# Optimization experiments

Measured on AMD Instinct MI355X. Metric: run time of the kernel, lower is better.

## Reference

```python
import jax, jax.numpy as jnp
import numpy as np

N_NODES = 50000
N_EDGES = 800000
D = 128
N_GRAPHS = 64


def setup_inputs() -> dict:
    key = jax.random.key(0)
    ks = jax.random.split(key, 10)
    x = jax.random.normal(ks[0], (N_NODES, D), dtype=jnp.float32)
    edge_weight = jax.random.uniform(ks[1], (N_EDGES,), dtype=jnp.float32)
    W1 = jax.random.normal(ks[2], (D, D), dtype=jnp.float32) / np.sqrt(D)
    b1 = jax.random.normal(ks[3], (D,), dtype=jnp.float32) * 0.01
    W2 = jax.random.normal(ks[4], (D, D), dtype=jnp.float32) / np.sqrt(D)
    b2 = jax.random.normal(ks[5], (D,), dtype=jnp.float32) * 0.01
    Wh = jax.random.normal(ks[6], (D, 1), dtype=jnp.float32) / np.sqrt(D)
    bh = jax.random.normal(ks[7], (1,), dtype=jnp.float32) * 0.01
    edge_index = jax.random.randint(ks[8], (2, N_EDGES), 0, N_NODES, dtype=jnp.int64)
    batch = jnp.sort(jax.random.randint(ks[9], (N_NODES,), 0, N_GRAPHS, dtype=jnp.int64))
    return {"x": x, "edge_weight": edge_weight, "W1": W1, "b1": b1,
            "W2": W2, "b2": b2, "Wh": Wh, "bh": bh,
            "edge_index": edge_index, "batch": batch}


def reference(x, edge_weight, W1, b1, W2, b2, Wh, bh, edge_index, batch):
    N = x.shape[0]
    # --- GCN normalization with self-loops (computed once; shared by layers) ---
    row, col = edge_index[0], edge_index[1]
    loop = jnp.arange(N, dtype=edge_index.dtype)
    row2 = jnp.concatenate([row, loop])   # source nodes
    col2 = jnp.concatenate([col, loop])   # target nodes
    ew2 = jnp.concatenate([edge_weight, jnp.ones((N,), dtype=x.dtype)])
    deg = jax.ops.segment_sum(ew2, col2, num_segments=N)
    dinv = jnp.where(deg > 0, jax.lax.rsqrt(deg), 0.0)
    norm = dinv[row2] * ew2 * dinv[col2]  # [E+N]

    def gcn_conv(h, W, b):
        h = h @ W                                   # [N, D_out]
        msg = norm[:, None] * h[row2]               # gather + scale, [E+N, D_out]
        return jax.ops.segment_sum(msg, col2, num_segments=N) + b

    # dropout is identity in eval mode
    h = jax.nn.relu(gcn_conv(x, W1, b1))
    h = jax.nn.relu(gcn_conv(h, W2, b2))

    # --- global mean pool over graphs ---
    counts = jax.ops.segment_sum(jnp.ones((N,), dtype=h.dtype), batch, num_segments=N_GRAPHS)
    pooled = jax.ops.segment_sum(h, batch, num_segments=N_GRAPHS)
    pooled = pooled / jnp.maximum(counts, 1.0)[:, None]
    return pooled @ Wh + bh
```

## Files before the change

### kernel.cpp

```cpp
#include <hip/hip_runtime.h>
#include <hip/hip_bf16.h>
#include <hip/hip_fp16.h>

#define N_NODES  50000
#define N_EDGES  800000
#define D        128
#define N_GRAPHS 64
#define CAP      64
#define EW_SCALE 1048576.0f
#define NB_GEMM1 391
#define NB_FILL  3125
#define NB_AGG16 3125

typedef _Float16 half8 __attribute__((ext_vector_type(8)));
typedef float   float4v __attribute__((ext_vector_type(4)));

__device__ __forceinline__ float2 h2f(unsigned int u) {
    __half2 h = *reinterpret_cast<__half2*>(&u);
    return __half22float2(h);
}
__device__ __forceinline__ unsigned int f2h(float a, float b) {
    __half2 h = __floats2half2_rn(a, b);
    return *reinterpret_cast<unsigned int*>(&h);
}
__device__ __forceinline__ float hu2f(unsigned short u) {
    __half_raw hr; hr.x = u;
    return __half2float(__half(hr));
}
__device__ __forceinline__ void unpack_pd(unsigned long long p, int& n, float& dv) {
    int c = (int)(p >> 40);
    n = c < CAP ? c : CAP;
    dv = rsqrtf(1.0f + (float)(p & 0xFFFFFFFFFFULL) * (1.0f / EW_SCALE));
}

__global__ __launch_bounds__(256) void fused_gemm1_fill(const float* __restrict__ X,
                                                        const float* __restrict__ W,
                                                        __half* __restrict__ Yh,
                                                        const int* __restrict__ ei,
                                                        const float* __restrict__ ew,
                                                        unsigned long long* __restrict__ packed,
                                                        unsigned int* __restrict__ bucket) {
    __shared__ float XT[32 * 128];
    __shared__ float Ws[32 * 128];

    if (blockIdx.x >= NB_GEMM1) {
        int e = (blockIdx.x - NB_GEMM1) * 256 + threadIdx.x;
        if (e >= N_EDGES) return;
        int r = ei[e];
        int c = ei[N_EDGES + e];
        float w = ew[e];
        unsigned long long add = (1ULL << 40) | (unsigned long long)(unsigned)(w * EW_SCALE + 0.5f);
        unsigned long long old = atomicAdd(&packed[c], add);
        unsigned pos = (unsigned)(old >> 40);
        if (pos < CAP) {
            unsigned short wh = __half_as_ushort(__float2half_rn(w));
            bucket[(size_t)c * CAP + pos] = (unsigned)r | ((unsigned)wh << 16);
        }
        return;
    }

    const int tid  = threadIdx.x;
    const int row0 = blockIdx.x * 128;
    const int tr = tid >> 4, tc = tid & 15;
    float acc[8][8] = {};

    for (int kt = 0; kt < 4; kt++) {
        const int kbase = kt * 32;
        {
            const float4* src = (const float4*)(W + kbase * 128);
            float4* dst = (float4*)Ws;
            for (int i = tid; i < 1024; i += 256) dst[i] = src[i];
        }
        {
            int r  = tid >> 1;
            int rr = row0 + r; if (rr >= N_NODES) rr = N_NODES - 1;
            int k0 = (tid & 1) * 16;
            const float4* src = (const float4*)(X + (size_t)rr * 128 + kbase + k0);
#pragma unroll
            for (int i = 0; i < 4; i++) {
                float4 v = src[i];
                int k = k0 + i * 4;
                XT[(k + 0) * 128 + r] = v.x;
                XT[(k + 1) * 128 + r] = v.y;
                XT[(k + 2) * 128 + r] = v.z;
                XT[(k + 3) * 128 + r] = v.w;
            }
        }
        __syncthreads();
#pragma unroll 4
        for (int k = 0; k < 32; k++) {
            float xs[8], ws[8];
            *(float4*)&xs[0] = *(const float4*)(XT + k * 128 + tr * 8);
            *(float4*)&xs[4] = *(const float4*)(XT + k * 128 + tr * 8 + 4);
            *(float4*)&ws[0] = *(const float4*)(Ws + k * 128 + tc * 8);
            *(float4*)&ws[4] = *(const float4*)(Ws + k * 128 + tc * 8 + 4);
#pragma unroll
            for (int i = 0; i < 8; i++)
#pragma unroll
                for (int j = 0; j < 8; j++)
                    acc[i][j] += xs[i] * ws[j];
        }
        __syncthreads();
    }
#pragma unroll
    for (int i = 0; i < 8; i++) {
        int r = row0 + tr * 8 + i;
        if (r < N_NODES) {
            uint4 p;
            p.x = f2h(acc[i][0], acc[i][1]);
            p.y = f2h(acc[i][2], acc[i][3]);
            p.z = f2h(acc[i][4], acc[i][5]);
            p.w = f2h(acc[i][6], acc[i][7]);
            *(uint4*)(Yh + (size_t)r * 128 + tc * 8) = p;
        }
    }
}

__global__ __launch_bounds__(512) void agg1_gemm2_kernel(const __half* __restrict__ xw1,
                                                         const unsigned long long* __restrict__ packed,
                                                         const unsigned int* __restrict__ bucket,
                                                         const float* __restrict__ b1,
                                                         const float* __restrict__ W2,
                                                         __half* __restrict__ x2) {
    __shared__ _Float16 sh1[16][136];
    const int wv   = threadIdx.x >> 6;
    const int lane = threadIdx.x & 63;
    const unsigned int* xh = (const unsigned int*)xw1;
    const int node0 = blockIdx.x * 16;

    float2 bb = ((const float2*)b1)[lane];

#pragma unroll
    for (int j = 0; j < 2; j++) {
        int node = node0 + wv * 2 + j;
        int n; float dv;
        unpack_pd(packed[node], n, dv);

        unsigned pk = 0u;
        if (lane < n) {
            unsigned eh = bucket[(size_t)node * CAP + lane];
            int src = eh & 0xFFFFu;
            int sn; float sdv;
            unpack_pd(packed[src], sn, sdv);
            float v = hu2f((unsigned short)(eh >> 16)) * sdv;
            pk = (unsigned)src | ((unsigned)__half_as_ushort(__float2half_rn(v)) << 16);
        }
        int pki = (int)pk;

        float2 xs = h2f(xh[(size_t)node * 64 + lane]);
        float accx = dv * xs.x;
        float accy = dv * xs.y;

        int i = 0;
        for (; i + 3 < n; i += 4) {
            unsigned v0u = (unsigned)__shfl(pki, i);
            unsigned v1u = (unsigned)__shfl(pki, i + 1);
            unsigned v2u = (unsigned)__shfl(pki, i + 2);
            unsigned v3u = (unsigned)__shfl(pki, i + 3);
            int r0 = v0u & 0xFFFF, r1 = v1u & 0xFFFF, r2 = v2u & 0xFFFF, r3 = v3u & 0xFFFF;
            float v0 = hu2f((unsigned short)(v0u >> 16));
            float v1 = hu2f((unsigned short)(v1u >> 16));
            float v2 = hu2f((unsigned short)(v2u >> 16));
            float v3 = hu2f((unsigned short)(v3u >> 16));
            float2 f0 = h2f(xh[(size_t)r0 * 64 + lane]);
            float2 f1 = h2f(xh[(size_t)r1 * 64 + lane]);
            float2 f2 = h2f(xh[(size_t)r2 * 64 + lane]);
            float2 f3 = h2f(xh[(size_t)r3 * 64 + lane]);
            accx += v0 * f0.x + v1 * f1.x + v2 * f2.x + v3 * f3.x;
            accy += v0 * f0.y + v1 * f1.y + v2 * f2.y + v3 * f3.y;
        }
        for (; i < n; i++) {
            unsigned v0u = (unsigned)__shfl(pki, i);
            int r0 = v0u & 0xFFFF;
            float v0 = hu2f((unsigned short)(v0u >> 16));
            float2 f0 = h2f(xh[(size_t)r0 * 64 + lane]);
            accx += v0 * f0.x;
            accy += v0 * f0.y;
        }

        float hx = fmaxf(dv * accx + bb.x, 0.0f);
        float hy = fmaxf(dv * accy + bb.y, 0.0f);
        int lr = wv * 2 + j;
        sh1[lr][lane * 2]     = (_Float16)hx;
        sh1[lr][lane * 2 + 1] = (_Float16)hy;
    }
    __syncthreads();

    const int quad = lane >> 4;
    const int l16  = lane & 15;
    float4v acc0 = {};
#pragma unroll
    for (int kc = 0; kc < 4; kc++) {
        const int k0 = kc * 32;
        half8 a = *(const half8*)(&sh1[l16][k0 + quad * 8]);
        const float* wp = W2 + (size_t)(k0 + quad * 8) * 128 + wv * 16 + l16;
        half8 b;
#pragma unroll
        for (int jj = 0; jj < 8; jj++) b[jj] = (_Float16)wp[jj * 128];
        acc0 = __builtin_amdgcn_mfma_f32_16x16x32_f16(a, b, acc0, 0, 0, 0);
    }
#pragma unroll
    for (int r = 0; r < 4; r++) {
        int row = node0 + quad * 4 + r;
        int rn; float s;
        unpack_pd(packed[row], rn, s);
        x2[(size_t)row * 128 + wv * 16 + l16] = __float2half_rn(acc0[r] * s);
    }
}

__global__ __launch_bounds__(256) void agg_head_kernel(const __half* __restrict__ xwh,
                                                       const unsigned long long* __restrict__ packed,
                                                       const unsigned int* __restrict__ bucket,
                                                       const float* __restrict__ bias,
                                                       const float* __restrict__ Wh,
                                                       float* __restrict__ nodedot) {
    int node = blockIdx.x * 4 + (threadIdx.x >> 6);
    int lane = threadIdx.x & 63;
    const unsigned int* xh = (const unsigned int*)xwh;

    int n; float dv;
    unpack_pd(packed[node], n, dv);

    unsigned int ehdr = (lane < n) ? bucket[(size_t)node * CAP + lane] : 0u;
    int eh = (int)ehdr;

    float2 xs = h2f(xh[(size_t)node * 64 + lane]);
    float accx = xs.x;
    float accy = xs.y;

    int i = 0;
    for (; i + 3 < n; i += 4) {
        unsigned v0u = (unsigned)__shfl(eh, i);
        unsigned v1u = (unsigned)__shfl(eh, i + 1);
        unsigned v2u = (unsigned)__shfl(eh, i + 2);
        unsigned v3u = (unsigned)__shfl(eh, i + 3);
        int r0 = v0u & 0xFFFF, r1 = v1u & 0xFFFF, r2 = v2u & 0xFFFF, r3 = v3u & 0xFFFF;
        float v0 = hu2f((unsigned short)(v0u >> 16));
        float v1 = hu2f((unsigned short)(v1u >> 16));
        float v2 = hu2f((unsigned short)(v2u >> 16));
        float v3 = hu2f((unsigned short)(v3u >> 16));
        float2 f0 = h2f(xh[(size_t)r0 * 64 + lane]);
        float2 f1 = h2f(xh[(size_t)r1 * 64 + lane]);
        float2 f2 = h2f(xh[(size_t)r2 * 64 + lane]);
        float2 f3 = h2f(xh[(size_t)r3 * 64 + lane]);
        accx += v0 * f0.x + v1 * f1.x + v2 * f2.x + v3 * f3.x;
        accy += v0 * f0.y + v1 * f1.y + v2 * f2.y + v3 * f3.y;
    }
    for (; i < n; i++) {
        unsigned v0u = (unsigned)__shfl(eh, i);
        int r0 = v0u & 0xFFFF;
        float v0 = hu2f((unsigned short)(v0u >> 16));
        float2 f0 = h2f(xh[(size_t)r0 * 64 + lane]);
        accx += v0 * f0.x;
        accy += v0 * f0.y;
    }

    float2 b = ((const float2*)bias)[lane];
    float hx = fmaxf(dv * accx + b.x, 0.0f);
    float hy = fmaxf(dv * accy + b.y, 0.0f);
    float2 w = ((const float2*)Wh)[lane];
    float s = hx * w.x + hy * w.y;
#pragma unroll
    for (int off = 32; off > 0; off >>= 1) s += __shfl_down(s, off, 64);
    if (lane == 0) nodedot[node] = s;
}

__global__ __launch_bounds__(256) void final2_kernel(const float* __restrict__ nodedot,
                                                     const int* __restrict__ batch,
                                                     const float* __restrict__ bh,
                                                     float* __restrict__ out) {
    __shared__ float red[256];
    int g = blockIdx.x;
    int lo = 0, hi = N_NODES;
    while (lo < hi) { int mid = (lo + hi) >> 1; if (batch[mid] < g) lo = mid + 1; else hi = mid; }
    int a = lo;
    hi = N_NODES;
    while (lo < hi) { int mid = (lo + hi) >> 1; if (batch[mid] < g + 1) lo = mid + 1; else hi = mid; }
    int b = lo;

    float s = 0.0f;
    for (int n = a + threadIdx.x; n < b; n += 256) s += nodedot[n];
    red[threadIdx.x] = s;
    __syncthreads();
#pragma unroll
    for (int off = 128; off > 0; off >>= 1) {
        if (threadIdx.x < off) red[threadIdx.x] += red[threadIdx.x + off];
        __syncthreads();
    }
    if (threadIdx.x == 0)
        out[g] = red[0] / fmaxf((float)(b - a), 1.0f) + bh[0];
}

extern "C" void kernel_launch(void* const* d_in, const int* in_sizes, int n_in,
                              void* d_out, int out_size, void* d_ws, size_t ws_size,
                              hipStream_t stream) {
    const float* x   = (const float*)d_in[0];
    const float* ew  = (const float*)d_in[1];
    const float* W1  = (const float*)d_in[2];
    const float* b1  = (const float*)d_in[3];
    const float* W2  = (const float*)d_in[4];
    const float* b2  = (const float*)d_in[5];
    const float* Wh  = (const float*)d_in[6];
    const float* bh  = (const float*)d_in[7];
    const int*   ei  = (const int*)d_in[8];
    const int*   bat = (const int*)d_in[9];
    float* out = (float*)d_out;

    char* ws = (char*)d_ws;
    __half* bufAh  = (__half*)ws;                         ws += (size_t)N_NODES * D * 2;
    __half* bufBh  = (__half*)ws;                         ws += (size_t)N_NODES * D * 2;
    unsigned int* bucket = (unsigned int*)ws;             ws += (size_t)N_NODES * CAP * 4;
    unsigned long long* packed = (unsigned long long*)ws; ws += (size_t)N_NODES * 8;
    float*  nodedot = (float*)ws;                         ws += (size_t)N_NODES * 4;

    const int nb_agg4 = N_NODES / 4;

    hipMemsetAsync(packed, 0, (size_t)N_NODES * 8, stream);

    fused_gemm1_fill<<<NB_GEMM1 + NB_FILL, 256, 0, stream>>>(x, W1, bufAh, ei, ew, packed, bucket);

    agg1_gemm2_kernel<<<NB_AGG16, 512, 0, stream>>>(bufAh, packed, bucket, b1, W2, bufBh);

    agg_head_kernel<<<nb_agg4, 256, 0, stream>>>(bufBh, packed, bucket, b2, Wh, nodedot);

    final2_kernel<<<N_GRAPHS, 256, 0, stream>>>(nodedot, bat, bh, out);
}
```

Measured before the change: 225.9 us.

## Use MFMA f16 for first GEMM and unroll gather loops by eight

The first GEMM, which used an FP32 shared-memory outer-product tile, now runs on MFMA 16x16x32 f16. Each wave handles 16 rows, converts X and W1 to half in registers, and uses no shared memory, so the GEMM block count doubles. Separately, both aggregation loops are unrolled from 4 to 8 neighbours to keep more gathers in flight. The costs are f16 rounding of X and W1 inputs, strided uncoalesced W loads repeated per wave, and more register pressure in the unrolled gathers.

```diff
diff --git a/kernel.cpp b/kernel.cpp
--- a/kernel.cpp
+++ b/kernel.cpp
@@ -8,7 +8,7 @@
 #define N_GRAPHS 64
 #define CAP      64
 #define EW_SCALE 1048576.0f
-#define NB_GEMM1 391
+#define NB_G1M   782
 #define NB_FILL  3125
 #define NB_AGG16 3125
 
@@ -18,10 +18,6 @@
 __device__ __forceinline__ float2 h2f(unsigned int u) {
     __half2 h = *reinterpret_cast<__half2*>(&u);
     return __half22float2(h);
-}
-__device__ __forceinline__ unsigned int f2h(float a, float b) {
-    __half2 h = __floats2half2_rn(a, b);
-    return *reinterpret_cast<unsigned int*>(&h);
 }
 __device__ __forceinline__ float hu2f(unsigned short u) {
     __half_raw hr; hr.x = u;
@@ -40,11 +36,8 @@
                                                         const float* __restrict__ ew,
                                                         unsigned long long* __restrict__ packed,
                                                         unsigned int* __restrict__ bucket) {
-    __shared__ float XT[32 * 128];
-    __shared__ float Ws[32 * 128];
-
-    if (blockIdx.x >= NB_GEMM1) {
-        int e = (blockIdx.x - NB_GEMM1) * 256 + threadIdx.x;
+    if (blockIdx.x >= NB_G1M) {
+        int e = (blockIdx.x - NB_G1M) * 256 + threadIdx.x;
         if (e >= N_EDGES) return;
         int r = ei[e];
         int c = ei[N_EDGES + e];
@@ -59,59 +52,40 @@
         return;
     }
 
-    const int tid  = threadIdx.x;
-    const int row0 = blockIdx.x * 128;
-    const int tr = tid >> 4, tc = tid & 15;
-    float acc[8][8] = {};
-
-    for (int kt = 0; kt < 4; kt++) {
-        const int kbase = kt * 32;
-        {
-            const float4* src = (const float4*)(W + kbase * 128);
-            float4* dst = (float4*)Ws;
-            for (int i = tid; i < 1024; i += 256) dst[i] = src[i];
-        }
-        {
-            int r  = tid >> 1;
-            int rr = row0 + r; if (rr >= N_NODES) rr = N_NODES - 1;
-            int k0 = (tid & 1) * 16;
-            const float4* src = (const float4*)(X + (size_t)rr * 128 + kbase + k0);
-#pragma unroll
-            for (int i = 0; i < 4; i++) {
-                float4 v = src[i];
-                int k = k0 + i * 4;
-                XT[(k + 0) * 128 + r] = v.x;
-                XT[(k + 1) * 128 + r] = v.y;
-                XT[(k + 2) * 128 + r] = v.z;
-                XT[(k + 3) * 128 + r] = v.w;
-            }
-        }
-        __syncthreads();
-#pragma unroll 4
-        for (int k = 0; k < 32; k++) {
-            float xs[8], ws[8];
-            *(float4*)&xs[0] = *(const float4*)(XT + k * 128 + tr * 8);
-            *(float4*)&xs[4] = *(const float4*)(XT + k * 128 + tr * 8 + 4);
-            *(float4*)&ws[0] = *(const float4*)(Ws + k * 128 + tc * 8);
-            *(float4*)&ws[4] = *(const float4*)(Ws + k * 128 + tc * 8 + 4);
-#pragma unroll
-            for (int i = 0; i < 8; i++)
-#pragma unroll
-                for (int j = 0; j < 8; j++)
-                    acc[i][j] += xs[i] * ws[j];
-        }
-        __syncthreads();
-    }
-#pragma unroll
-    for (int i = 0; i < 8; i++) {
-        int r = row0 + tr * 8 + i;
-        if (r < N_NODES) {
-            uint4 p;
-            p.x = f2h(acc[i][0], acc[i][1]);
-            p.y = f2h(acc[i][2], acc[i][3]);
-            p.z = f2h(acc[i][4], acc[i][5]);
-            p.w = f2h(acc[i][6], acc[i][7]);
-            *(uint4*)(Yh + (size_t)r * 128 + tc * 8) = p;
+    const int wv   = threadIdx.x >> 6;
+    const int lane = threadIdx.x & 63;
+    const int quad = lane >> 4;
+    const int l16  = lane & 15;
+    const int row0 = blockIdx.x * 64 + wv * 16;
+    if (row0 >= N_NODES) return;
+
+    float4v acc[8] = {};
+#pragma unroll
+    for (int kc = 0; kc < 4; kc++) {
+        const int k0 = kc * 32;
+        const float* xp = X + (size_t)(row0 + l16) * 128 + k0 + quad * 8;
+        float4 a0 = *(const float4*)xp;
+        float4 a1 = *(const float4*)(xp + 4);
+        half8 a;
+        a[0] = (_Float16)a0.x; a[1] = (_Float16)a0.y;
+        a[2] = (_Float16)a0.z; a[3] = (_Float16)a0.w;
+        a[4] = (_Float16)a1.x; a[5] = (_Float16)a1.y;
+        a[6] = (_Float16)a1.z; a[7] = (_Float16)a1.w;
+#pragma unroll
+        for (int ct = 0; ct < 8; ct++) {
+            const float* wp = W + (size_t)(k0 + quad * 8) * 128 + ct * 16 + l16;
+            half8 b;
+#pragma unroll
+            for (int j = 0; j < 8; j++) b[j] = (_Float16)wp[j * 128];
+            acc[ct] = __builtin_amdgcn_mfma_f32_16x16x32_f16(a, b, acc[ct], 0, 0, 0);
+        }
+    }
+#pragma unroll
+    for (int r = 0; r < 4; r++) {
+        int row = row0 + quad * 4 + r;
+#pragma unroll
+        for (int ct = 0; ct < 8; ct++) {
+            Yh[(size_t)row * 128 + ct * 16 + l16] = __float2half_rn(acc[ct][r]);
         }
     }
 }
@@ -152,28 +126,40 @@
         float accy = dv * xs.y;
 
         int i = 0;
-        for (; i + 3 < n; i += 4) {
-            unsigned v0u = (unsigned)__shfl(pki, i);
-            unsigned v1u = (unsigned)__shfl(pki, i + 1);
-            unsigned v2u = (unsigned)__shfl(pki, i + 2);
-            unsigned v3u = (unsigned)__shfl(pki, i + 3);
-            int r0 = v0u & 0xFFFF, r1 = v1u & 0xFFFF, r2 = v2u & 0xFFFF, r3 = v3u & 0xFFFF;
-            float v0 = hu2f((unsigned short)(v0u >> 16));
-            float v1 = hu2f((unsigned short)(v1u >> 16));
-            float v2 = hu2f((unsigned short)(v2u >> 16));
-            float v3 = hu2f((unsigned short)(v3u >> 16));
-            float2 f0 = h2f(xh[(size_t)r0 * 64 + lane]);
-            float2 f1 = h2f(xh[(size_t)r1 * 64 + lane]);
-            float2 f2 = h2f(xh[(size_t)r2 * 64 + lane]);
-            float2 f3 = h2f(xh[(size_t)r3 * 64 + lane]);
-            accx += v0 * f0.x + v1 * f1.x + v2 * f2.x + v3 * f3.x;
-            accy += v0 * f0.y + v1 * f1.y + v2 * f2.y + v3 * f3.y;
+        for (; i + 7 < n; i += 8) {
+            unsigned u0 = (unsigned)__shfl(pki, i);
+            unsigned u1 = (unsigned)__shfl(pki, i + 1);
+            unsigned u2 = (unsigned)__shfl(pki, i + 2);
+            unsigned u3 = (unsigned)__shfl(pki, i + 3);
+            unsigned u4 = (unsigned)__shfl(pki, i + 4);
+            unsigned u5 = (unsigned)__shfl(pki, i + 5);
+            unsigned u6 = (unsigned)__shfl(pki, i + 6);
+            unsigned u7 = (unsigned)__shfl(pki, i + 7);
+            float2 f0 = h2f(xh[(size_t)(u0 & 0xFFFF) * 64 + lane]);
+            float2 f1 = h2f(xh[(size_t)(u1 & 0xFFFF) * 64 + lane]);
+            float2 f2 = h2f(xh[(size_t)(u2 & 0xFFFF) * 64 + lane]);
+            float2 f3 = h2f(xh[(size_t)(u3 & 0xFFFF) * 64 + lane]);
+            float2 f4 = h2f(xh[(size_t)(u4 & 0xFFFF) * 64 + lane]);
+            float2 f5 = h2f(xh[(size_t)(u5 & 0xFFFF) * 64 + lane]);
+            float2 f6 = h2f(xh[(size_t)(u6 & 0xFFFF) * 64 + lane]);
+            float2 f7 = h2f(xh[(size_t)(u7 & 0xFFFF) * 64 + lane]);
+            float v0 = hu2f((unsigned short)(u0 >> 16));
+            float v1 = hu2f((unsigned short)(u1 >> 16));
+            float v2 = hu2f((unsigned short)(u2 >> 16));
+            float v3 = hu2f((unsigned short)(u3 >> 16));
+            float v4 = hu2f((unsigned short)(u4 >> 16));
+            float v5 = hu2f((unsigned short)(u5 >> 16));
+            float v6 = hu2f((unsigned short)(u6 >> 16));
+            float v7 = hu2f((unsigned short)(u7 >> 16));
+            accx += v0*f0.x + v1*f1.x + v2*f2.x + v3*f3.x
+                  + v4*f4.x + v5*f5.x + v6*f6.x + v7*f7.x;
+            accy += v0*f0.y + v1*f1.y + v2*f2.y + v3*f3.y
+                  + v4*f4.y + v5*f5.y + v6*f6.y + v7*f7.y;
         }
         for (; i < n; i++) {
-            unsigned v0u = (unsigned)__shfl(pki, i);
-            int r0 = v0u & 0xFFFF;
-            float v0 = hu2f((unsigned short)(v0u >> 16));
-            float2 f0 = h2f(xh[(size_t)r0 * 64 + lane]);
+            unsigned u0 = (unsigned)__shfl(pki, i);
+            float v0 = hu2f((unsigned short)(u0 >> 16));
+            float2 f0 = h2f(xh[(size_t)(u0 & 0xFFFF) * 64 + lane]);
             accx += v0 * f0.x;
             accy += v0 * f0.y;
         }
@@ -229,28 +215,40 @@
     float accy = xs.y;
 
     int i = 0;
-    for (; i + 3 < n; i += 4) {
-        unsigned v0u = (unsigned)__shfl(eh, i);
-        unsigned v1u = (unsigned)__shfl(eh, i + 1);
-        unsigned v2u = (unsigned)__shfl(eh, i + 2);
-        unsigned v3u = (unsigned)__shfl(eh, i + 3);
-        int r0 = v0u & 0xFFFF, r1 = v1u & 0xFFFF, r2 = v2u & 0xFFFF, r3 = v3u & 0xFFFF;
-        float v0 = hu2f((unsigned short)(v0u >> 16));
-        float v1 = hu2f((unsigned short)(v1u >> 16));
-        float v2 = hu2f((unsigned short)(v2u >> 16));
-        float v3 = hu2f((unsigned short)(v3u >> 16));
-        float2 f0 = h2f(xh[(size_t)r0 * 64 + lane]);
-        float2 f1 = h2f(xh[(size_t)r1 * 64 + lane]);
-        float2 f2 = h2f(xh[(size_t)r2 * 64 + lane]);
-        float2 f3 = h2f(xh[(size_t)r3 * 64 + lane]);
-        accx += v0 * f0.x + v1 * f1.x + v2 * f2.x + v3 * f3.x;
-        accy += v0 * f0.y + v1 * f1.y + v2 * f2.y + v3 * f3.y;
+    for (; i + 7 < n; i += 8) {
+        unsigned u0 = (unsigned)__shfl(eh, i);
+        unsigned u1 = (unsigned)__shfl(eh, i + 1);
+        unsigned u2 = (unsigned)__shfl(eh, i + 2);
+        unsigned u3 = (unsigned)__shfl(eh, i + 3);
+        unsigned u4 = (unsigned)__shfl(eh, i + 4);
+        unsigned u5 = (unsigned)__shfl(eh, i + 5);
+        unsigned u6 = (unsigned)__shfl(eh, i + 6);
+        unsigned u7 = (unsigned)__shfl(eh, i + 7);
+        float2 f0 = h2f(xh[(size_t)(u0 & 0xFFFF) * 64 + lane]);
+        float2 f1 = h2f(xh[(size_t)(u1 & 0xFFFF) * 64 + lane]);
+        float2 f2 = h2f(xh[(size_t)(u2 & 0xFFFF) * 64 + lane]);
+        float2 f3 = h2f(xh[(size_t)(u3 & 0xFFFF) * 64 + lane]);
+        float2 f4 = h2f(xh[(size_t)(u4 & 0xFFFF) * 64 + lane]);
+        float2 f5 = h2f(xh[(size_t)(u5 & 0xFFFF) * 64 + lane]);
+        float2 f6 = h2f(xh[(size_t)(u6 & 0xFFFF) * 64 + lane]);
+        float2 f7 = h2f(xh[(size_t)(u7 & 0xFFFF) * 64 + lane]);
+        float v0 = hu2f((unsigned short)(u0 >> 16));
+        float v1 = hu2f((unsigned short)(u1 >> 16));
+        float v2 = hu2f((unsigned short)(u2 >> 16));
+        float v3 = hu2f((unsigned short)(u3 >> 16));
+        float v4 = hu2f((unsigned short)(u4 >> 16));
+        float v5 = hu2f((unsigned short)(u5 >> 16));
+        float v6 = hu2f((unsigned short)(u6 >> 16));
+        float v7 = hu2f((unsigned short)(u7 >> 16));
+        accx += v0*f0.x + v1*f1.x + v2*f2.x + v3*f3.x
+              + v4*f4.x + v5*f5.x + v6*f6.x + v7*f7.x;
+        accy += v0*f0.y + v1*f1.y + v2*f2.y + v3*f3.y
+              + v4*f4.y + v5*f5.y + v6*f6.y + v7*f7.y;
     }
     for (; i < n; i++) {
-        unsigned v0u = (unsigned)__shfl(eh, i);
-        int r0 = v0u & 0xFFFF;
-        float v0 = hu2f((unsigned short)(v0u >> 16));
-        float2 f0 = h2f(xh[(size_t)r0 * 64 + lane]);
+        unsigned u0 = (unsigned)__shfl(eh, i);
+        float v0 = hu2f((unsigned short)(u0 >> 16));
+        float2 f0 = h2f(xh[(size_t)(u0 & 0xFFFF) * 64 + lane]);
         accx += v0 * f0.x;
         accy += v0 * f0.y;
     }
@@ -317,7 +315,7 @@
 
     hipMemsetAsync(packed, 0, (size_t)N_NODES * 8, stream);
 
-    fused_gemm1_fill<<<NB_GEMM1 + NB_FILL, 256, 0, stream>>>(x, W1, bufAh, ei, ew, packed, bucket);
+    fused_gemm1_fill<<<NB_G1M + NB_FILL, 256, 0, stream>>>(x, W1, bufAh, ei, ew, packed, bucket);
 
     agg1_gemm2_kernel<<<NB_AGG16, 512, 0, stream>>>(bufAh, packed, bucket, b1, W2, bufBh);
 
```

Result: no change. 229.3 us (+1.5%).
